# Optimization experiments

Measured on AMD Instinct MI355X. Metric: run time of the kernel, lower is better.

Reference implementation:

```python
import jax, jax.numpy as jnp
import numpy as np
import math

# --- delta-LFIT rule-space combinatorics ---
NUM_VARS, DELAYS = 3, 3
N = NUM_VARS * DELAYS  # 9 delayed variables

def delta_count(l, n):
    # number of rule bodies of length exactly l: choose l of n vars, each with a polarity
    return math.comb(n, l) * (2 ** l)

MAX_RULE_LEN = max(delta_count(l, N) for l in range(N + 1))  # 5376
OUT_DIM = MAX_RULE_LEN + 1  # padded logits + trailing 'empty rule' logit
N_HEADS = N + 1  # rules_pred has heads for rule_len = 0..N

B, S = 512, 1
DIM_IN = 1024
DIM_HIDDEN = 1024
LAYERS = 4  # -> LAYERS+1 Linear layers total (no nonlinearity in the original Sequential)


def setup_inputs() -> dict:
    key = jax.random.key(0)
    ks = jax.random.split(key, 4)
    latent = jax.random.normal(ks[0], (B, S, DIM_IN), dtype=jnp.float32)
    rule_len = jax.random.randint(ks[1], (B,), 0, N_HEADS, dtype=jnp.int32)

    n_lin = LAYERS + 1  # dim_in==dim_hidden so all trunk linears stack uniformly
    scale = 1.0 / np.sqrt(DIM_HIDDEN)
    W_mlp = jax.random.normal(ks[2], (n_lin, DIM_HIDDEN, DIM_HIDDEN), dtype=jnp.float32) * scale
    b_mlp = jnp.zeros((n_lin, DIM_HIDDEN), dtype=jnp.float32)

    # Padded head weight bank: row layout matches torch.cat((out[..., :-1], zeros_pad, out[..., -1:]))
    rng = np.random.default_rng(0)
    Wh = np.zeros((N_HEADS, OUT_DIM, DIM_HIDDEN), dtype=np.float32)
    bh = np.zeros((N_HEADS, OUT_DIM), dtype=np.float32)
    for l in range(N_HEADS):
        d = delta_count(l, N) + 1  # head l output dim: length(l)-length(l-1)+1
        w = (rng.standard_normal((d, DIM_HIDDEN)) * scale).astype(np.float32)
        b = (rng.standard_normal(d) * 0.01).astype(np.float32)
        Wh[l, : d - 1] = w[:-1]
        Wh[l, OUT_DIM - 1] = w[-1]
        bh[l, : d - 1] = b[:-1]
        bh[l, OUT_DIM - 1] = b[-1]

    return {
        "latent": latent,
        "W_mlp": W_mlp,
        "b_mlp": b_mlp,
        "W_heads": jnp.asarray(Wh),
        "b_heads": jnp.asarray(bh),
        "rule_len": rule_len,
    }


def reference(latent, W_mlp, b_mlp, W_heads, b_heads, rule_len):
    # Trunk: stack of Linear layers, no activation (matches the original Sequential)
    h = latent  # [B, S, H]
    for i in range(W_mlp.shape[0]):
        h = h @ W_mlp[i].T + b_mlp[i]
    # Per-sample dynamic head dispatch (rule_len_is_diff=True branch), vectorized:
    # compute all padded heads, then gather each sample's head.
    all_out = jnp.einsum('bsh,loh->bslo', h, W_heads) + b_heads  # [B, S, N_HEADS, OUT_DIM]
    idx = rule_len.astype(jnp.int32)[:, None, None, None]  # [B,1,1,1]
    out = jnp.take_along_axis(all_out, idx, axis=2)[:, :, 0, :]  # [B, S, OUT_DIM]
    return out
```

## Files before the change

### kernel.cpp

```cpp
#include <hip/hip_runtime.h>

#define DIM     1024
#define BATCH   512
#define OUTD    5377
#define NHEADS  10
#define NLAYERS 5

typedef __attribute__((ext_vector_type(4))) float f32x4;
typedef __attribute__((ext_vector_type(8))) short bf16x8;

__device__ __forceinline__ unsigned short f2bf(float f) {
    unsigned u = __builtin_bit_cast(unsigned, f);
    u = (u + 0x7FFFu + ((u >> 16) & 1u)) >> 16;
    return (unsigned short)u;
}
__device__ __forceinline__ float bf2f(unsigned short h) {
    unsigned u = ((unsigned)h) << 16;
    return __builtin_bit_cast(float, u);
}

__global__ void group_kernel(const int* __restrict__ rule_len,
                             int* __restrict__ bidx,
                             int* __restrict__ gstart,
                             int* __restrict__ gcount) {
    __shared__ int s_count[NHEADS];
    __shared__ int s_fill[NHEADS];
    int t = threadIdx.x;
    if (t < NHEADS) s_count[t] = 0;
    __syncthreads();
    int h = rule_len[t];
    atomicAdd(&s_count[h], 1);
    __syncthreads();
    if (t == 0) {
        int acc = 0;
        for (int i = 0; i < NHEADS; ++i) {
            gstart[i] = acc;
            gcount[i] = s_count[i];
            s_fill[i] = acc;
            acc += s_count[i];
        }
    }
    __syncthreads();
    int pos = atomicAdd(&s_fill[h], 1);
    bidx[pos] = t;
}

__global__ void convert_latent(const float* __restrict__ in,
                               unsigned short* __restrict__ out) {
    int i = blockIdx.x * blockDim.x + threadIdx.x;
    float4 v = ((const float4*)in)[i];
    ushort4 o;
    o.x = f2bf(v.x); o.y = f2bf(v.y); o.z = f2bf(v.z); o.w = f2bf(v.w);
    ((ushort4*)out)[i] = o;
}

#define LDK 72

__global__ __launch_bounds__(256) void mlp_mfma(
    const unsigned short* __restrict__ A,
    const float* __restrict__ W,
    const float* __restrict__ bias,
    unsigned short* __restrict__ C)
{
    __shared__ __align__(16) unsigned short As[32][LDK];
    __shared__ __align__(16) unsigned short Whi[32][LDK];
    __shared__ __align__(16) unsigned short Wlo[32][LDK];

    const int tid = threadIdx.x;
    const int n0 = blockIdx.x * 32;
    const int m0 = blockIdx.y * 32;
    const int lane = tid & 63;
    const int wid = tid >> 6;
    const int wm = (wid >> 1) * 16;
    const int wn = (wid & 1) * 16;

    f32x4 acc = {0.f, 0.f, 0.f, 0.f};

    const int ar = tid >> 3;
    const int ac = (tid & 7) * 8;
    const int wr = tid >> 4;
    const int wc = (tid & 15) * 4;

    const unsigned short* Ap = A + (size_t)(m0 + ar) * DIM + ac;
    const float* Wp0 = W + (size_t)(n0 + wr) * DIM + wc;
    const float* Wp1 = W + (size_t)(n0 + wr + 16) * DIM + wc;

    for (int k0 = 0; k0 < DIM; k0 += 64) {
        *(uint4*)&As[ar][ac] = *(const uint4*)(Ap + k0);
        {
            float4 w = *(const float4*)(Wp0 + k0);
            ushort4 hi, lo;
            hi.x = f2bf(w.x); lo.x = f2bf(w.x - bf2f(hi.x));
            hi.y = f2bf(w.y); lo.y = f2bf(w.y - bf2f(hi.y));
            hi.z = f2bf(w.z); lo.z = f2bf(w.z - bf2f(hi.z));
            hi.w = f2bf(w.w); lo.w = f2bf(w.w - bf2f(hi.w));
            *(ushort4*)&Whi[wr][wc] = hi;
            *(ushort4*)&Wlo[wr][wc] = lo;
        }
        {
            float4 w = *(const float4*)(Wp1 + k0);
            ushort4 hi, lo;
            hi.x = f2bf(w.x); lo.x = f2bf(w.x - bf2f(hi.x));
            hi.y = f2bf(w.y); lo.y = f2bf(w.y - bf2f(hi.y));
            hi.z = f2bf(w.z); lo.z = f2bf(w.z - bf2f(hi.z));
            hi.w = f2bf(w.w); lo.w = f2bf(w.w - bf2f(hi.w));
            *(ushort4*)&Whi[wr + 16][wc] = hi;
            *(ushort4*)&Wlo[wr + 16][wc] = lo;
        }
        __syncthreads();
        #pragma unroll
        for (int kk = 0; kk < 2; ++kk) {
            const int ko = kk * 32 + (lane >> 4) * 8;
            bf16x8 a  = *(const bf16x8*)&As[wm + (lane & 15)][ko];
            bf16x8 bh = *(const bf16x8*)&Whi[wn + (lane & 15)][ko];
            bf16x8 bl = *(const bf16x8*)&Wlo[wn + (lane & 15)][ko];
            acc = __builtin_amdgcn_mfma_f32_16x16x32_bf16(a, bh, acc, 0, 0, 0);
            acc = __builtin_amdgcn_mfma_f32_16x16x32_bf16(a, bl, acc, 0, 0, 0);
        }
        __syncthreads();
    }

    const int cn = n0 + wn + (lane & 15);
    const float bn = bias[cn];
    const int rbase = m0 + wm + (lane >> 4) * 4;
    #pragma unroll
    for (int j = 0; j < 4; ++j) {
        C[(size_t)(rbase + j) * DIM + cn] = f2bf(acc[j] + bn);
    }
}

__global__ __launch_bounds__(256) void head_mfma(
    const unsigned short* __restrict__ H,
    const float* __restrict__ Wh,
    const float* __restrict__ bh,
    const int* __restrict__ bidx,
    const int* __restrict__ gstart,
    const int* __restrict__ gcount,
    float* __restrict__ out)
{
    const int head = blockIdx.z;
    const int cnt = gcount[head];
    const int m0 = blockIdx.y * 64;
    if (m0 >= cnt) return;
    const int n0 = blockIdx.x * 64;

    __shared__ __align__(16) unsigned short As[64][LDK];
    __shared__ __align__(16) unsigned short Whi[64][LDK];
    __shared__ __align__(16) unsigned short Wlo[64][LDK];
    __shared__ int s_b[64];

    const int tid = threadIdx.x;
    if (tid < 64) {
        int mi = m0 + tid;
        s_b[tid] = (mi < cnt) ? bidx[gstart[head] + mi] : -1;
    }
    __syncthreads();

    const int lane = tid & 63;
    const int wid = tid >> 6;
    const int wm = (wid >> 1) * 32;
    const int wn = (wid & 1) * 32;

    f32x4 acc[2][2] = {};

    const int ar = tid >> 3;
    const int ac = (tid & 7) * 8;
    int b0 = s_b[ar];       if (b0 < 0) b0 = 0;
    int b1 = s_b[ar + 32];  if (b1 < 0) b1 = 0;
    const unsigned short* Ap0 = H + (size_t)b0 * DIM + ac;
    const unsigned short* Ap1 = H + (size_t)b1 * DIM + ac;

    const int wr = tid >> 4;
    const int wc = (tid & 15) * 4;
    const float* WhL = Wh + (size_t)head * OUTD * DIM;
    const float* Wp[4];
    #pragma unroll
    for (int p = 0; p < 4; ++p) {
        int r = n0 + wr + p * 16;
        if (r > OUTD - 1) r = OUTD - 1;
        Wp[p] = WhL + (size_t)r * DIM + wc;
    }

    for (int k0 = 0; k0 < DIM; k0 += 64) {
        *(uint4*)&As[ar][ac]      = *(const uint4*)(Ap0 + k0);
        *(uint4*)&As[ar + 32][ac] = *(const uint4*)(Ap1 + k0);
        #pragma unroll
        for (int p = 0; p < 4; ++p) {
            float4 w = *(const float4*)(Wp[p] + k0);
            ushort4 hi, lo;
            hi.x = f2bf(w.x); lo.x = f2bf(w.x - bf2f(hi.x));
            hi.y = f2bf(w.y); lo.y = f2bf(w.y - bf2f(hi.y));
            hi.z = f2bf(w.z); lo.z = f2bf(w.z - bf2f(hi.z));
            hi.w = f2bf(w.w); lo.w = f2bf(w.w - bf2f(hi.w));
            *(ushort4*)&Whi[wr + p * 16][wc] = hi;
            *(ushort4*)&Wlo[wr + p * 16][wc] = lo;
        }
        __syncthreads();
        #pragma unroll
        for (int kk = 0; kk < 2; ++kk) {
            const int ko = kk * 32 + (lane >> 4) * 8;
            bf16x8 a0 = *(const bf16x8*)&As[wm + (lane & 15)][ko];
            bf16x8 a1 = *(const bf16x8*)&As[wm + 16 + (lane & 15)][ko];
            bf16x8 h0 = *(const bf16x8*)&Whi[wn + (lane & 15)][ko];
            bf16x8 h1 = *(const bf16x8*)&Whi[wn + 16 + (lane & 15)][ko];
            bf16x8 l0 = *(const bf16x8*)&Wlo[wn + (lane & 15)][ko];
            bf16x8 l1 = *(const bf16x8*)&Wlo[wn + 16 + (lane & 15)][ko];
            acc[0][0] = __builtin_amdgcn_mfma_f32_16x16x32_bf16(a0, h0, acc[0][0], 0, 0, 0);
            acc[0][0] = __builtin_amdgcn_mfma_f32_16x16x32_bf16(a0, l0, acc[0][0], 0, 0, 0);
            acc[0][1] = __builtin_amdgcn_mfma_f32_16x16x32_bf16(a0, h1, acc[0][1], 0, 0, 0);
            acc[0][1] = __builtin_amdgcn_mfma_f32_16x16x32_bf16(a0, l1, acc[0][1], 0, 0, 0);
            acc[1][0] = __builtin_amdgcn_mfma_f32_16x16x32_bf16(a1, h0, acc[1][0], 0, 0, 0);
            acc[1][0] = __builtin_amdgcn_mfma_f32_16x16x32_bf16(a1, l0, acc[1][0], 0, 0, 0);
            acc[1][1] = __builtin_amdgcn_mfma_f32_16x16x32_bf16(a1, h1, acc[1][1], 0, 0, 0);
            acc[1][1] = __builtin_amdgcn_mfma_f32_16x16x32_bf16(a1, l1, acc[1][1], 0, 0, 0);
        }
        __syncthreads();
    }

    const float* bhL = bh + (size_t)head * OUTD;
    #pragma unroll
    for (int fm = 0; fm < 2; ++fm) {
        #pragma unroll
        for (int fn = 0; fn < 2; ++fn) {
            int n = n0 + wn + fn * 16 + (lane & 15);
            if (n >= OUTD) continue;
            float bn = bhL[n];
            #pragma unroll
            for (int j = 0; j < 4; ++j) {
                int mi = wm + fm * 16 + (lane >> 4) * 4 + j;
                int b = s_b[mi];
                if (b >= 0) out[(size_t)b * OUTD + n] = acc[fm][fn][j] + bn;
            }
        }
    }
}

extern "C" void kernel_launch(void* const* d_in, const int* in_sizes, int n_in,
                              void* d_out, int out_size, void* d_ws, size_t ws_size,
                              hipStream_t stream) {
    const float* latent   = (const float*)d_in[0];
    const float* W_mlp    = (const float*)d_in[1];
    const float* b_mlp    = (const float*)d_in[2];
    const float* W_heads  = (const float*)d_in[3];
    const float* b_heads  = (const float*)d_in[4];
    const int*   rule_len = (const int*)d_in[5];
    float* out = (float*)d_out;

    unsigned short* h0 = (unsigned short*)d_ws;
    unsigned short* h1 = h0 + (size_t)BATCH * DIM;
    int* bidx   = (int*)(h1 + (size_t)BATCH * DIM);
    int* gstart = bidx + BATCH;
    int* gcount = gstart + 16;

    group_kernel<<<1, BATCH, 0, stream>>>(rule_len, bidx, gstart, gcount);

    convert_latent<<<(BATCH * DIM / 4) / 256, 256, 0, stream>>>(latent, h0);

    dim3 mgrid(DIM / 32, BATCH / 32);
    const unsigned short* src = h0;
    unsigned short* dst = h1;
    for (int l = 0; l < NLAYERS; ++l) {
        mlp_mfma<<<mgrid, 256, 0, stream>>>(src,
                                            W_mlp + (size_t)l * DIM * DIM,
                                            b_mlp + (size_t)l * DIM,
                                            dst);
        const unsigned short* t = dst;
        dst = (unsigned short*)(src == h0 ? h0 : h1);
        dst = (dst == h0) ? h1 : h0;
        dst = (unsigned short*)((t == h0) ? h1 : h0);
        src = t;
    }

    dim3 hgrid((OUTD + 63) / 64, BATCH / 64, NHEADS);
    head_mfma<<<hgrid, 256, 0, stream>>>(src, W_heads, b_heads,
                                         bidx, gstart, gcount, out);
}
```

Before: 139.1 us.

## Double-buffer LDS tiles with register prefetch and drop lo-split in head GEMM

Both GEMM kernels now prefetch the next K-tile from global memory into registers while computing on a double-buffered shared-memory tile, removing the trailing barrier per iteration. The head kernel also stops splitting weights into bf16 hi/lo pairs and uses only the rounded bf16 weight, halving MFMA work and LDS traffic there. This lowers accuracy of the head output and raises register pressure from the prefetch buffers.

```diff
diff --git a/kernel.cpp b/kernel.cpp
--- a/kernel.cpp
+++ b/kernel.cpp
@@ -5,6 +5,7 @@
 #define OUTD    5377
 #define NHEADS  10
 #define NLAYERS 5
+#define LDK     72
 
 typedef __attribute__((ext_vector_type(4))) float f32x4;
 typedef __attribute__((ext_vector_type(8))) short bf16x8;
@@ -54,17 +55,15 @@
     ((ushort4*)out)[i] = o;
 }
 
-#define LDK 72
-
 __global__ __launch_bounds__(256) void mlp_mfma(
     const unsigned short* __restrict__ A,
     const float* __restrict__ W,
     const float* __restrict__ bias,
     unsigned short* __restrict__ C)
 {
-    __shared__ __align__(16) unsigned short As[32][LDK];
-    __shared__ __align__(16) unsigned short Whi[32][LDK];
-    __shared__ __align__(16) unsigned short Wlo[32][LDK];
+    __shared__ __align__(16) unsigned short As[2][32][LDK];
+    __shared__ __align__(16) unsigned short Whi[2][32][LDK];
+    __shared__ __align__(16) unsigned short Wlo[2][32][LDK];
 
     const int tid = threadIdx.x;
     const int n0 = blockIdx.x * 32;
@@ -85,39 +84,44 @@
     const float* Wp0 = W + (size_t)(n0 + wr) * DIM + wc;
     const float* Wp1 = W + (size_t)(n0 + wr + 16) * DIM + wc;
 
-    for (int k0 = 0; k0 < DIM; k0 += 64) {
-        *(uint4*)&As[ar][ac] = *(const uint4*)(Ap + k0);
+    uint4  ra  = *(const uint4*)(Ap);
+    float4 rw0 = *(const float4*)(Wp0);
+    float4 rw1 = *(const float4*)(Wp1);
+
+    for (int t = 0; t < DIM / 64; ++t) {
+        const int cur = t & 1;
+        *(uint4*)&As[cur][ar][ac] = ra;
         {
-            float4 w = *(const float4*)(Wp0 + k0);
             ushort4 hi, lo;
-            hi.x = f2bf(w.x); lo.x = f2bf(w.x - bf2f(hi.x));
-            hi.y = f2bf(w.y); lo.y = f2bf(w.y - bf2f(hi.y));
-            hi.z = f2bf(w.z); lo.z = f2bf(w.z - bf2f(hi.z));
-            hi.w = f2bf(w.w); lo.w = f2bf(w.w - bf2f(hi.w));
-            *(ushort4*)&Whi[wr][wc] = hi;
-            *(ushort4*)&Wlo[wr][wc] = lo;
-        }
-        {
-            float4 w = *(const float4*)(Wp1 + k0);
-            ushort4 hi, lo;
-            hi.x = f2bf(w.x); lo.x = f2bf(w.x - bf2f(hi.x));
-            hi.y = f2bf(w.y); lo.y = f2bf(w.y - bf2f(hi.y));
-            hi.z = f2bf(w.z); lo.z = f2bf(w.z - bf2f(hi.z));
-            hi.w = f2bf(w.w); lo.w = f2bf(w.w - bf2f(hi.w));
-            *(ushort4*)&Whi[wr + 16][wc] = hi;
-            *(ushort4*)&Wlo[wr + 16][wc] = lo;
+            hi.x = f2bf(rw0.x); lo.x = f2bf(rw0.x - bf2f(hi.x));
+            hi.y = f2bf(rw0.y); lo.y = f2bf(rw0.y - bf2f(hi.y));
+            hi.z = f2bf(rw0.z); lo.z = f2bf(rw0.z - bf2f(hi.z));
+            hi.w = f2bf(rw0.w); lo.w = f2bf(rw0.w - bf2f(hi.w));
+            *(ushort4*)&Whi[cur][wr][wc] = hi;
+            *(ushort4*)&Wlo[cur][wr][wc] = lo;
+            hi.x = f2bf(rw1.x); lo.x = f2bf(rw1.x - bf2f(hi.x));
+            hi.y = f2bf(rw1.y); lo.y = f2bf(rw1.y - bf2f(hi.y));
+            hi.z = f2bf(rw1.z); lo.z = f2bf(rw1.z - bf2f(hi.z));
+            hi.w = f2bf(rw1.w); lo.w = f2bf(rw1.w - bf2f(hi.w));
+            *(ushort4*)&Whi[cur][wr + 16][wc] = hi;
+            *(ushort4*)&Wlo[cur][wr + 16][wc] = lo;
         }
         __syncthreads();
+        if (t < DIM / 64 - 1) {
+            const int k0 = (t + 1) * 64;
+            ra  = *(const uint4*)(Ap + k0);
+            rw0 = *(const float4*)(Wp0 + k0);
+            rw1 = *(const float4*)(Wp1 + k0);
+        }
         #pragma unroll
         for (int kk = 0; kk < 2; ++kk) {
             const int ko = kk * 32 + (lane >> 4) * 8;
-            bf16x8 a  = *(const bf16x8*)&As[wm + (lane & 15)][ko];
-            bf16x8 bh = *(const bf16x8*)&Whi[wn + (lane & 15)][ko];
-            bf16x8 bl = *(const bf16x8*)&Wlo[wn + (lane & 15)][ko];
+            bf16x8 a  = *(const bf16x8*)&As[cur][wm + (lane & 15)][ko];
+            bf16x8 bh = *(const bf16x8*)&Whi[cur][wn + (lane & 15)][ko];
+            bf16x8 bl = *(const bf16x8*)&Wlo[cur][wn + (lane & 15)][ko];
             acc = __builtin_amdgcn_mfma_f32_16x16x32_bf16(a, bh, acc, 0, 0, 0);
             acc = __builtin_amdgcn_mfma_f32_16x16x32_bf16(a, bl, acc, 0, 0, 0);
         }
-        __syncthreads();
     }
 
     const int cn = n0 + wn + (lane & 15);
@@ -144,9 +148,8 @@
     if (m0 >= cnt) return;
     const int n0 = blockIdx.x * 64;
 
-    __shared__ __align__(16) unsigned short As[64][LDK];
-    __shared__ __align__(16) unsigned short Whi[64][LDK];
-    __shared__ __align__(16) unsigned short Wlo[64][LDK];
+    __shared__ __align__(16) unsigned short As[2][64][LDK];
+    __shared__ __align__(16) unsigned short Ws[2][64][LDK];
     __shared__ int s_b[64];
 
     const int tid = threadIdx.x;
@@ -181,40 +184,45 @@
         Wp[p] = WhL + (size_t)r * DIM + wc;
     }
 
-    for (int k0 = 0; k0 < DIM; k0 += 64) {
-        *(uint4*)&As[ar][ac]      = *(const uint4*)(Ap0 + k0);
-        *(uint4*)&As[ar + 32][ac] = *(const uint4*)(Ap1 + k0);
+    uint4 ra0 = *(const uint4*)(Ap0);
+    uint4 ra1 = *(const uint4*)(Ap1);
+    float4 rw[4];
+    #pragma unroll
+    for (int p = 0; p < 4; ++p) rw[p] = *(const float4*)(Wp[p]);
+
+    for (int t = 0; t < DIM / 64; ++t) {
+        const int cur = t & 1;
+        *(uint4*)&As[cur][ar][ac]      = ra0;
+        *(uint4*)&As[cur][ar + 32][ac] = ra1;
         #pragma unroll
         for (int p = 0; p < 4; ++p) {
-            float4 w = *(const float4*)(Wp[p] + k0);
-            ushort4 hi, lo;
-            hi.x = f2bf(w.x); lo.x = f2bf(w.x - bf2f(hi.x));
-            hi.y = f2bf(w.y); lo.y = f2bf(w.y - bf2f(hi.y));
-            hi.z = f2bf(w.z); lo.z = f2bf(w.z - bf2f(hi.z));
-            hi.w = f2bf(w.w); lo.w = f2bf(w.w - bf2f(hi.w));
-            *(ushort4*)&Whi[wr + p * 16][wc] = hi;
-            *(ushort4*)&Wlo[wr + p * 16][wc] = lo;
+            ushort4 hi;
+            hi.x = f2bf(rw[p].x);
+            hi.y = f2bf(rw[p].y);
+            hi.z = f2bf(rw[p].z);
+            hi.w = f2bf(rw[p].w);
+            *(ushort4*)&Ws[cur][wr + p * 16][wc] = hi;
         }
         __syncthreads();
+        if (t < DIM / 64 - 1) {
+            const int k0 = (t + 1) * 64;
+            ra0 = *(const uint4*)(Ap0 + k0);
+            ra1 = *(const uint4*)(Ap1 + k0);
+            #pragma unroll
+            for (int p = 0; p < 4; ++p) rw[p] = *(const float4*)(Wp[p] + k0);
+        }
         #pragma unroll
         for (int kk = 0; kk < 2; ++kk) {
             const int ko = kk * 32 + (lane >> 4) * 8;
-            bf16x8 a0 = *(const bf16x8*)&As[wm + (lane & 15)][ko];
-            bf16x8 a1 = *(const bf16x8*)&As[wm + 16 + (lane & 15)][ko];
-            bf16x8 h0 = *(const bf16x8*)&Whi[wn + (lane & 15)][ko];
-            bf16x8 h1 = *(const bf16x8*)&Whi[wn + 16 + (lane & 15)][ko];
-            bf16x8 l0 = *(const bf16x8*)&Wlo[wn + (lane & 15)][ko];
-            bf16x8 l1 = *(const bf16x8*)&Wlo[wn + 16 + (lane & 15)][ko];
-            acc[0][0] = __builtin_amdgcn_mfma_f32_16x16x32_bf16(a0, h0, acc[0][0], 0, 0, 0);
-            acc[0][0] = __builtin_amdgcn_mfma_f32_16x16x32_bf16(a0, l0, acc[0][0], 0, 0, 0);
-            acc[0][1] = __builtin_amdgcn_mfma_f32_16x16x32_bf16(a0, h1, acc[0][1], 0, 0, 0);
-            acc[0][1] = __builtin_amdgcn_mfma_f32_16x16x32_bf16(a0, l1, acc[0][1], 0, 0, 0);
-            acc[1][0] = __builtin_amdgcn_mfma_f32_16x16x32_bf16(a1, h0, acc[1][0], 0, 0, 0);
-            acc[1][0] = __builtin_amdgcn_mfma_f32_16x16x32_bf16(a1, l0, acc[1][0], 0, 0, 0);
-            acc[1][1] = __builtin_amdgcn_mfma_f32_16x16x32_bf16(a1, h1, acc[1][1], 0, 0, 0);
-            acc[1][1] = __builtin_amdgcn_mfma_f32_16x16x32_bf16(a1, l1, acc[1][1], 0, 0, 0);
-        }
-        __syncthreads();
+            bf16x8 a0 = *(const bf16x8*)&As[cur][wm + (lane & 15)][ko];
+            bf16x8 a1 = *(const bf16x8*)&As[cur][wm + 16 + (lane & 15)][ko];
+            bf16x8 w0 = *(const bf16x8*)&Ws[cur][wn + (lane & 15)][ko];
+            bf16x8 w1 = *(const bf16x8*)&Ws[cur][wn + 16 + (lane & 15)][ko];
+            acc[0][0] = __builtin_amdgcn_mfma_f32_16x16x32_bf16(a0, w0, acc[0][0], 0, 0, 0);
+            acc[0][1] = __builtin_amdgcn_mfma_f32_16x16x32_bf16(a0, w1, acc[0][1], 0, 0, 0);
+            acc[1][0] = __builtin_amdgcn_mfma_f32_16x16x32_bf16(a1, w0, acc[1][0], 0, 0, 0);
+            acc[1][1] = __builtin_amdgcn_mfma_f32_16x16x32_bf16(a1, w1, acc[1][1], 0, 0, 0);
+        }
     }
 
     const float* bhL = bh + (size_t)head * OUTD;
@@ -253,7 +261,6 @@
     int* gcount = gstart + 16;
 
     group_kernel<<<1, BATCH, 0, stream>>>(rule_len, bidx, gstart, gcount);
-
     convert_latent<<<(BATCH * DIM / 4) / 256, 256, 0, stream>>>(latent, h0);
 
     dim3 mgrid(DIM / 32, BATCH / 32);
@@ -264,11 +271,9 @@
                                             W_mlp + (size_t)l * DIM * DIM,
                                             b_mlp + (size_t)l * DIM,
                                             dst);
-        const unsigned short* t = dst;
-        dst = (unsigned short*)(src == h0 ? h0 : h1);
-        dst = (dst == h0) ? h1 : h0;
-        dst = (unsigned short*)((t == h0) ? h1 : h0);
-        src = t;
+        const unsigned short* t = src;
+        src = dst;
+        dst = (unsigned short*)t;
     }
 
     dim3 hgrid((OUTD + 63) / 64, BATCH / 64, NHEADS);
```

Result: faster. 123.0 us (-11.5%).
